# Kernel tuning notes

Hardware: AMD Instinct MI355X
Metric: run time of the kernel (lower is better)

Reference implementation:

```python
import jax, jax.numpy as jnp
import numpy as np

B, N, D, H = 32, 2048, 65, 64  # batch, seq_len, in_dim+out_dim, hid
GAMMA = 0.0001


def setup_inputs() -> dict:
    key = jax.random.key(0)
    kx, kq, kk, kv = jax.random.split(key, 4)
    x = jax.random.normal(kx, (B, N, D), dtype=jnp.float32)
    std_qk = (GAMMA / D) ** 0.5
    Wq = jax.random.normal(kq, (H, D), dtype=jnp.float32) * std_qk
    Wk = jax.random.normal(kk, (H, D), dtype=jnp.float32) * std_qk
    Wv = jax.random.normal(kv, (D, D), dtype=jnp.float32) * GAMMA
    return {"x": x, "Wq": Wq, "Wk": Wk, "Wv": Wv}


def reference(x, Wq, Wk, Wv):
    # Linear projections (torch nn.Linear: x @ W^T)
    Q = jnp.einsum('bnd,hd->bnh', x, Wq)  # [B, N, H]
    K = jnp.einsum('bnd,hd->bnh', x, Wk)  # [B, N, H]
    V = jnp.einsum('bnd,ed->bne', x, Wv)  # [B, N, D]
    # Non-softmax linear attention: (Q K^T) V, as written in the module
    scores = jnp.einsum('bnh,bmh->bnm', Q, K)  # [B, N, N]
    out = jnp.einsum('bnm,bmd->bnd', scores, V)  # [B, N, D]
    return out
```

## Files before the change

kernel.cpp:

```cpp
#include <hip/hip_runtime.h>

#define BB 32
#define NN 2048
#define DD 65
#define HH 64
#define ST 68
#define TILE (DD * ST)
#define CC 32

__device__ __forceinline__ float4 f4add(float4 a, float4 b) {
  return make_float4(a.x + b.x, a.y + b.y, a.z + b.z, a.w + b.w);
}

#define GL2LDS(g, l)                                             \
  __builtin_amdgcn_global_load_lds(                              \
      (const __attribute__((address_space(1))) void*)(g),        \
      (__attribute__((address_space(3))) void*)(l), 16, 0, 0)

__global__ __launch_bounds__(128, 2) void k1_gram(const float* __restrict__ x,
                                                  float* __restrict__ P) {
  __shared__ __align__(16) float Xl[2][64 * ST];
  const int t = (int)threadIdx.x;
  const int w = t >> 6, lane = t & 63;
  const int tx8 = lane & 7, ty8 = lane >> 3;
  const int chunk = (int)blockIdx.x * 2 + w;
  const int b = chunk >> 5, c = chunk & 31;
  const float4* src4 =
      (const float4*)(x + ((size_t)b * NN + (size_t)c * 64) * DD);
  float* Xw = Xl[w];

#pragma unroll
  for (int p = 0; p < 2; p++) {
    float4 tmp[9];
    const int cnt = p ? 8 : 9;
#pragma unroll
    for (int q = 0; q < 9; q++) {
      const int i4 = lane + 64 * (9 * p + q);
      if (q < cnt && i4 < 1040) tmp[q] = src4[i4];
    }
#pragma unroll
    for (int q = 0; q < 9; q++) {
      const int i4 = lane + 64 * (9 * p + q);
      if (q < cnt && i4 < 1040) {
        const int f = 4 * i4;
        const float vv[4] = {tmp[q].x, tmp[q].y, tmp[q].z, tmp[q].w};
#pragma unroll
        for (int j = 0; j < 4; j++) {
          const int r = (f + j) / DD, cc = (f + j) - r * DD;
          Xw[r * ST + cc] = vv[j];
        }
      }
    }
  }

  float g[8][8] = {};
  float f64[8] = {};
  float gcc = 0.f;
  for (int n = 0; n < 64; n++) {
    float rowf[8], colf[8];
    *(float4*)&rowf[0] = *(const float4*)&Xw[n * ST + 8 * ty8];
    *(float4*)&rowf[4] = *(const float4*)&Xw[n * ST + 8 * ty8 + 4];
    *(float4*)&colf[0] = *(const float4*)&Xw[n * ST + 8 * tx8];
    *(float4*)&colf[4] = *(const float4*)&Xw[n * ST + 8 * tx8 + 4];
    const float x64 = Xw[n * ST + 64];
#pragma unroll
    for (int r = 0; r < 8; r++)
#pragma unroll
      for (int cc = 0; cc < 8; cc++)
        g[r][cc] = fmaf(rowf[r], colf[cc], g[r][cc]);
#pragma unroll
    for (int cc = 0; cc < 8; cc++) f64[cc] = fmaf(x64, colf[cc], f64[cc]);
    gcc = fmaf(x64, x64, gcc);
  }

  float* Pp = P + (size_t)chunk * TILE;
#pragma unroll
  for (int r = 0; r < 8; r++) {
    *(float4*)&Pp[(8 * ty8 + r) * ST + 8 * tx8] = *(float4*)&g[r][0];
    *(float4*)&Pp[(8 * ty8 + r) * ST + 8 * tx8 + 4] = *(float4*)&g[r][4];
  }
  if (ty8 == 0) {
#pragma unroll
    for (int cc = 0; cc < 8; cc++) {
      Pp[64 * ST + 8 * tx8 + cc] = f64[cc];
      Pp[(8 * tx8 + cc) * ST + 64] = f64[cc];
    }
    if (tx8 == 0) Pp[64 * ST + 64] = gcc;
  }
}

__global__ __launch_bounds__(256) void kred(const float* __restrict__ P,
                                            float* __restrict__ G) {
  const int t = (int)threadIdx.x;
  const int blk = (int)blockIdx.x;
  const int b = blk / 5, s = blk - b * 5;
  const int Q = TILE / 4;
  const int i4 = s * 256 + t;
  if (i4 < Q) {
    const float4* Pb = (const float4*)(P + (size_t)b * CC * TILE);
    float4 acc = make_float4(0.f, 0.f, 0.f, 0.f);
#pragma unroll
    for (int grp = 0; grp < 4; grp++) {
      float4 v[8];
#pragma unroll
      for (int cc = 0; cc < 8; cc++)
        v[cc] = Pb[(size_t)(8 * grp + cc) * Q + i4];
#pragma unroll
      for (int stp = 4; stp >= 1; stp >>= 1)
#pragma unroll
        for (int cc = 0; cc < stp; cc++) v[cc] = f4add(v[cc], v[cc + stp]);
      acc = f4add(acc, v[0]);
    }
    ((float4*)(G + (size_t)b * TILE))[i4] = acc;
  }
}

__global__ __launch_bounds__(256) void k2_chain(
    const float* __restrict__ Wq, const float* __restrict__ Wk,
    const float* __restrict__ Wv, const float* __restrict__ G,
    float* __restrict__ Tm) {
  __shared__ __align__(16) float WqL[HH * ST];
  __shared__ __align__(16) float WkL[HH * ST];
  __shared__ __align__(16) float GL[TILE];
  __shared__ __align__(16) float WvT[TILE];
  __shared__ __align__(16) float Mr[8 * ST];
  __shared__ __align__(16) float Rr[8 * ST];

  const int t = (int)threadIdx.x;
  const int tx = t & 31, ty = t >> 5;
  const int blk = (int)blockIdx.x;
  const int b = blk / 9, rg = blk - b * 9;
  const int i = 8 * rg + ty;
  const bool alive = (i < DD);
  const int ic = alive ? i : 0;

  {
    float tq[17], tk[17];
#pragma unroll
    for (int q = 0; q < 17; q++) {
      const int idx = t + 256 * q;
      if (idx < HH * DD) { tq[q] = Wq[idx]; tk[q] = Wk[idx]; }
    }
#pragma unroll
    for (int q = 0; q < 17; q++) {
      const int idx = t + 256 * q;
      if (idx < HH * DD) {
        const int r = idx / DD, cc = idx - r * DD;
        WqL[r * ST + cc] = tq[q];
        WkL[r * ST + cc] = tk[q];
      }
    }
  }
  {
    const float4* Gb4 = (const float4*)(G + (size_t)b * TILE);
    float4 tG[5];
#pragma unroll
    for (int q = 0; q < 5; q++) {
      const int i4 = t + 256 * q;
      if (i4 < TILE / 4) tG[q] = Gb4[i4];
    }
#pragma unroll
    for (int q = 0; q < 5; q++) {
      const int i4 = t + 256 * q;
      if (i4 < TILE / 4) *((float4*)GL + i4) = tG[q];
    }
  }
  {
    float tv[17];
#pragma unroll
    for (int q = 0; q < 17; q++) {
      const int idx = t + 256 * q;
      if (idx < DD * DD) tv[q] = Wv[idx];
    }
#pragma unroll
    for (int q = 0; q < 17; q++) {
      const int idx = t + 256 * q;
      if (idx < DD * DD) {
        const int j = idx / DD, k = idx - j * DD;
        WvT[k * ST + j] = tv[q];
      }
    }
  }
  __syncthreads();

  {
    float m0 = 0.f, m1 = 0.f, m2 = 0.f;
    for (int h = 0; h < HH; h++) {
      const float wq = WqL[h * ST + ic];
      m0 = fmaf(wq, WkL[h * ST + tx], m0);
      m1 = fmaf(wq, WkL[h * ST + tx + 32], m1);
      m2 = fmaf(wq, WkL[h * ST + 64], m2);
    }
    if (alive) {
      Mr[ty * ST + tx] = m0;
      Mr[ty * ST + tx + 32] = m1;
      if (tx == 0) Mr[ty * ST + 64] = m2;
    }
  }
  __syncthreads();

  {
    float r0 = 0.f, r1 = 0.f, r2 = 0.f;
    for (int k = 0; k < DD; k++) {
      const float mm = Mr[ty * ST + k];
      r0 = fmaf(mm, GL[k * ST + tx], r0);
      r1 = fmaf(mm, GL[k * ST + tx + 32], r1);
      r2 = fmaf(mm, GL[k * ST + 64], r2);
    }
    if (alive) {
      Rr[ty * ST + tx] = r0;
      Rr[ty * ST + tx + 32] = r1;
      if (tx == 0) Rr[ty * ST + 64] = r2;
    }
  }
  __syncthreads();

  {
    float t0 = 0.f, t1 = 0.f, t2 = 0.f;
    for (int k = 0; k < DD; k++) {
      const float rv = Rr[ty * ST + k];
      t0 = fmaf(rv, WvT[k * ST + tx], t0);
      t1 = fmaf(rv, WvT[k * ST + tx + 32], t1);
      t2 = fmaf(rv, WvT[k * ST + 64], t2);
    }
    if (alive) {
      float* Tb = Tm + (size_t)b * TILE + (size_t)i * ST;
      Tb[tx] = t0;
      Tb[tx + 32] = t1;
      if (tx == 0) Tb[64] = t2;
    }
  }
}

__global__ __launch_bounds__(128, 2) void k3_out(const float* __restrict__ x,
                                                 const float* __restrict__ Tt,
                                                 float* __restrict__ out) {
  __shared__ __align__(16) float Tl[TILE];
  __shared__ __align__(16) float Xl[2][64 * ST];
  const int t = (int)threadIdx.x;
  const int w = t >> 6, lane = t & 63;
  const int tx8 = lane & 7, ty8 = lane >> 3;
  const int blk = (int)blockIdx.x;
  const int b = blk >> 4;
  const int chunk = (blk & 15) * 2 + w;
  const float4* Tg4 = (const float4*)(Tt + (size_t)b * TILE);
  const float4* src4 =
      (const float4*)(x + ((size_t)b * NN + (size_t)chunk * 64) * DD);
  float* Xw = Xl[w];

#pragma unroll
  for (int q = 0; q < 8; q++)
    GL2LDS(Tg4 + q * 128 + w * 64 + lane,
           Tl + (size_t)(q * 128 + w * 64) * 4);
  {
    const int s = 1024 + w * 64 + lane;
    if (s < TILE / 4) GL2LDS(Tg4 + s, Tl + (size_t)(1024 + w * 64) * 4);
  }

#pragma unroll
  for (int p = 0; p < 2; p++) {
    float4 tmp[9];
    const int cnt = p ? 8 : 9;
#pragma unroll
    for (int q = 0; q < 9; q++) {
      const int i4 = lane + 64 * (9 * p + q);
      if (q < cnt && i4 < 1040) tmp[q] = src4[i4];
    }
#pragma unroll
    for (int q = 0; q < 9; q++) {
      const int i4 = lane + 64 * (9 * p + q);
      if (q < cnt && i4 < 1040) {
        const int f = 4 * i4;
        const float vv[4] = {tmp[q].x, tmp[q].y, tmp[q].z, tmp[q].w};
#pragma unroll
        for (int j = 0; j < 4; j++) {
          const int r = (f + j) / DD, cc = (f + j) - r * DD;
          Xw[r * ST + cc] = vv[j];
        }
      }
    }
  }
  __syncthreads();

  float o[8][8] = {}, o64[8] = {};
  for (int kk = 0; kk < 64; kk += 4) {
    float xa[8][4];
#pragma unroll
    for (int r = 0; r < 8; r++)
      *(float4*)xa[r] = *(const float4*)&Xw[(8 * ty8 + r) * ST + kk];
#pragma unroll
    for (int e = 0; e < 4; e++) {
      float tb[8];
      *(float4*)&tb[0] = *(const float4*)&Tl[(kk + e) * ST + 8 * tx8];
      *(float4*)&tb[4] = *(const float4*)&Tl[(kk + e) * ST + 8 * tx8 + 4];
      const float t64 = Tl[(kk + e) * ST + 64];
#pragma unroll
      for (int r = 0; r < 8; r++) {
#pragma unroll
        for (int cc = 0; cc < 8; cc++)
          o[r][cc] = fmaf(xa[r][e], tb[cc], o[r][cc]);
        o64[r] = fmaf(xa[r][e], t64, o64[r]);
      }
    }
  }
  {
    float tb[8];
    *(float4*)&tb[0] = *(const float4*)&Tl[64 * ST + 8 * tx8];
    *(float4*)&tb[4] = *(const float4*)&Tl[64 * ST + 8 * tx8 + 4];
    const float t64 = Tl[64 * ST + 64];
#pragma unroll
    for (int r = 0; r < 8; r++) {
      const float xs = Xw[(8 * ty8 + r) * ST + 64];
#pragma unroll
      for (int cc = 0; cc < 8; cc++)
        o[r][cc] = fmaf(xs, tb[cc], o[r][cc]);
      o64[r] = fmaf(xs, t64, o64[r]);
    }
  }

  float* Ow = Xw;
#pragma unroll
  for (int r = 0; r < 8; r++) {
#pragma unroll
    for (int cc = 0; cc < 8; cc++)
      Ow[(8 * ty8 + r) * DD + 8 * tx8 + cc] = o[r][cc];
    if (tx8 == 0) Ow[(8 * ty8 + r) * DD + 64] = o64[r];
  }
  float4* ob4 = (float4*)(out + ((size_t)b * NN + (size_t)chunk * 64) * DD);
#pragma unroll
  for (int q = 0; q < 17; q++) {
    const int i4 = lane + 64 * q;
    if (i4 < 1040) ob4[i4] = ((const float4*)Ow)[i4];
  }
}

extern "C" void kernel_launch(void* const* d_in, const int* in_sizes, int n_in,
                              void* d_out, int out_size, void* d_ws,
                              size_t ws_size, hipStream_t stream) {
  const float* x = (const float*)d_in[0];
  const float* Wq = (const float*)d_in[1];
  const float* Wk = (const float*)d_in[2];
  const float* Wv = (const float*)d_in[3];
  float* out = (float*)d_out;

  float* P = (float*)d_ws;
  float* G = P + (size_t)BB * CC * TILE;
  float* Tm = G + (size_t)BB * TILE;

  k1_gram<<<BB * CC / 2, 128, 0, stream>>>(x, P);
  kred<<<BB * 5, 256, 0, stream>>>(P, G);
  k2_chain<<<BB * 9, 256, 0, stream>>>(Wq, Wk, Wv, G, Tm);
  k3_out<<<BB * CC / 2, 128, 0, stream>>>(x, Tm, out);
  (void)in_sizes; (void)n_in; (void)out_size; (void)ws_size;
}
```

Measured before the change: 127.8 us.

## Halve row chunks to 32, use 4-wave blocks, read x directly in output kernel

The Gram partial kernel now processes 32-row chunks with four waves per block, doubling the number of partial tiles and the reduction depth in kred. The output kernel drops the LDS staging of x and the LDS-based output transpose. Each lane reads its four x rows straight from global memory and writes results directly with unaligned scalar stores. The aim is more waves in flight and less LDS use per block, at the cost of a heavier partial-sum write and reduce and uncoalesced scalar global loads and stores in k3.

```diff
diff --git a/kernel.cpp b/kernel.cpp
--- a/kernel.cpp
+++ b/kernel.cpp
@@ -6,7 +6,8 @@
 #define HH 64
 #define ST 68
 #define TILE (DD * ST)
-#define CC 32
+#define CH 64
+#define CROWS 32
 
 __device__ __forceinline__ float4 f4add(float4 a, float4 b) {
   return make_float4(a.x + b.x, a.y + b.y, a.z + b.z, a.w + b.w);
@@ -17,31 +18,29 @@
       (const __attribute__((address_space(1))) void*)(g),        \
       (__attribute__((address_space(3))) void*)(l), 16, 0, 0)
 
-__global__ __launch_bounds__(128, 2) void k1_gram(const float* __restrict__ x,
+__global__ __launch_bounds__(256, 4) void k1_gram(const float* __restrict__ x,
                                                   float* __restrict__ P) {
-  __shared__ __align__(16) float Xl[2][64 * ST];
+  __shared__ __align__(16) float Xl[4][CROWS * ST];
   const int t = (int)threadIdx.x;
   const int w = t >> 6, lane = t & 63;
   const int tx8 = lane & 7, ty8 = lane >> 3;
-  const int chunk = (int)blockIdx.x * 2 + w;
-  const int b = chunk >> 5, c = chunk & 31;
+  const int ch = (int)blockIdx.x * 4 + w;
+  const int b = ch >> 6, c = ch & 63;
   const float4* src4 =
-      (const float4*)(x + ((size_t)b * NN + (size_t)c * 64) * DD);
+      (const float4*)(x + ((size_t)b * NN + (size_t)c * CROWS) * DD);
   float* Xw = Xl[w];
 
-#pragma unroll
-  for (int p = 0; p < 2; p++) {
+  {
     float4 tmp[9];
-    const int cnt = p ? 8 : 9;
 #pragma unroll
     for (int q = 0; q < 9; q++) {
-      const int i4 = lane + 64 * (9 * p + q);
-      if (q < cnt && i4 < 1040) tmp[q] = src4[i4];
+      const int i4 = lane + 64 * q;
+      if (i4 < 520) tmp[q] = src4[i4];
     }
 #pragma unroll
     for (int q = 0; q < 9; q++) {
-      const int i4 = lane + 64 * (9 * p + q);
-      if (q < cnt && i4 < 1040) {
+      const int i4 = lane + 64 * q;
+      if (i4 < 520) {
         const int f = 4 * i4;
         const float vv[4] = {tmp[q].x, tmp[q].y, tmp[q].z, tmp[q].w};
 #pragma unroll
@@ -56,7 +55,7 @@
   float g[8][8] = {};
   float f64[8] = {};
   float gcc = 0.f;
-  for (int n = 0; n < 64; n++) {
+  for (int n = 0; n < CROWS; n++) {
     float rowf[8], colf[8];
     *(float4*)&rowf[0] = *(const float4*)&Xw[n * ST + 8 * ty8];
     *(float4*)&rowf[4] = *(const float4*)&Xw[n * ST + 8 * ty8 + 4];
@@ -73,7 +72,7 @@
     gcc = fmaf(x64, x64, gcc);
   }
 
-  float* Pp = P + (size_t)chunk * TILE;
+  float* Pp = P + (size_t)ch * TILE;
 #pragma unroll
   for (int r = 0; r < 8; r++) {
     *(float4*)&Pp[(8 * ty8 + r) * ST + 8 * tx8] = *(float4*)&g[r][0];
@@ -97,10 +96,10 @@
   const int Q = TILE / 4;
   const int i4 = s * 256 + t;
   if (i4 < Q) {
-    const float4* Pb = (const float4*)(P + (size_t)b * CC * TILE);
+    const float4* Pb = (const float4*)(P + (size_t)b * CH * TILE);
     float4 acc = make_float4(0.f, 0.f, 0.f, 0.f);
 #pragma unroll
-    for (int grp = 0; grp < 4; grp++) {
+    for (int grp = 0; grp < 8; grp++) {
       float4 v[8];
 #pragma unroll
       for (int cc = 0; cc < 8; cc++)
@@ -232,70 +231,53 @@
   }
 }
 
-__global__ __launch_bounds__(128, 2) void k3_out(const float* __restrict__ x,
+__global__ __launch_bounds__(256, 4) void k3_out(const float* __restrict__ x,
                                                  const float* __restrict__ Tt,
                                                  float* __restrict__ out) {
   __shared__ __align__(16) float Tl[TILE];
-  __shared__ __align__(16) float Xl[2][64 * ST];
   const int t = (int)threadIdx.x;
   const int w = t >> 6, lane = t & 63;
-  const int tx8 = lane & 7, ty8 = lane >> 3;
+  const int tx8 = lane & 7, ry4 = lane >> 3;
   const int blk = (int)blockIdx.x;
   const int b = blk >> 4;
-  const int chunk = (blk & 15) * 2 + w;
+  const int c = (blk & 15) * 4 + w;
   const float4* Tg4 = (const float4*)(Tt + (size_t)b * TILE);
-  const float4* src4 =
-      (const float4*)(x + ((size_t)b * NN + (size_t)chunk * 64) * DD);
-  float* Xw = Xl[w];
-
-#pragma unroll
-  for (int q = 0; q < 8; q++)
-    GL2LDS(Tg4 + q * 128 + w * 64 + lane,
-           Tl + (size_t)(q * 128 + w * 64) * 4);
+  const float* xs = x + ((size_t)b * NN + (size_t)c * CROWS) * DD;
+
+#pragma unroll
+  for (int q = 0; q < 4; q++)
+    GL2LDS(Tg4 + q * 256 + w * 64 + lane,
+           Tl + (size_t)(q * 256 + w * 64) * 4);
   {
     const int s = 1024 + w * 64 + lane;
     if (s < TILE / 4) GL2LDS(Tg4 + s, Tl + (size_t)(1024 + w * 64) * 4);
   }
-
-#pragma unroll
-  for (int p = 0; p < 2; p++) {
-    float4 tmp[9];
-    const int cnt = p ? 8 : 9;
-#pragma unroll
-    for (int q = 0; q < 9; q++) {
-      const int i4 = lane + 64 * (9 * p + q);
-      if (q < cnt && i4 < 1040) tmp[q] = src4[i4];
-    }
-#pragma unroll
-    for (int q = 0; q < 9; q++) {
-      const int i4 = lane + 64 * (9 * p + q);
-      if (q < cnt && i4 < 1040) {
-        const int f = 4 * i4;
-        const float vv[4] = {tmp[q].x, tmp[q].y, tmp[q].z, tmp[q].w};
-#pragma unroll
-        for (int j = 0; j < 4; j++) {
-          const int r = (f + j) / DD, cc = (f + j) - r * DD;
-          Xw[r * ST + cc] = vv[j];
-        }
-      }
-    }
-  }
   __syncthreads();
 
-  float o[8][8] = {}, o64[8] = {};
+  const float* xr0 = xs + (size_t)(4 * ry4 + 0) * DD;
+  const float* xr1 = xs + (size_t)(4 * ry4 + 1) * DD;
+  const float* xr2 = xs + (size_t)(4 * ry4 + 2) * DD;
+  const float* xr3 = xs + (size_t)(4 * ry4 + 3) * DD;
+
+  float o[4][8] = {}, o64[4] = {};
   for (int kk = 0; kk < 64; kk += 4) {
-    float xa[8][4];
-#pragma unroll
-    for (int r = 0; r < 8; r++)
-      *(float4*)xa[r] = *(const float4*)&Xw[(8 * ty8 + r) * ST + kk];
+    float xa[4][4];
 #pragma unroll
     for (int e = 0; e < 4; e++) {
+      xa[0][e] = xr0[kk + e];
+      xa[1][e] = xr1[kk + e];
+      xa[2][e] = xr2[kk + e];
+      xa[3][e] = xr3[kk + e];
+    }
+#pragma unroll
+    for (int e = 0; e < 4; e++) {
+      const int k = kk + e;
       float tb[8];
-      *(float4*)&tb[0] = *(const float4*)&Tl[(kk + e) * ST + 8 * tx8];
-      *(float4*)&tb[4] = *(const float4*)&Tl[(kk + e) * ST + 8 * tx8 + 4];
-      const float t64 = Tl[(kk + e) * ST + 64];
-#pragma unroll
-      for (int r = 0; r < 8; r++) {
+      *(float4*)&tb[0] = *(const float4*)&Tl[k * ST + 8 * tx8];
+      *(float4*)&tb[4] = *(const float4*)&Tl[k * ST + 8 * tx8 + 4];
+      const float t64 = Tl[k * ST + 64];
+#pragma unroll
+      for (int r = 0; r < 4; r++) {
 #pragma unroll
         for (int cc = 0; cc < 8; cc++)
           o[r][cc] = fmaf(xa[r][e], tb[cc], o[r][cc]);
@@ -304,33 +286,33 @@
     }
   }
   {
+    float xk[4];
+    xk[0] = xr0[64]; xk[1] = xr1[64]; xk[2] = xr2[64]; xk[3] = xr3[64];
     float tb[8];
     *(float4*)&tb[0] = *(const float4*)&Tl[64 * ST + 8 * tx8];
     *(float4*)&tb[4] = *(const float4*)&Tl[64 * ST + 8 * tx8 + 4];
     const float t64 = Tl[64 * ST + 64];
 #pragma unroll
-    for (int r = 0; r < 8; r++) {
-      const float xs = Xw[(8 * ty8 + r) * ST + 64];
+    for (int r = 0; r < 4; r++) {
 #pragma unroll
       for (int cc = 0; cc < 8; cc++)
-        o[r][cc] = fmaf(xs, tb[cc], o[r][cc]);
-      o64[r] = fmaf(xs, t64, o64[r]);
-    }
-  }
-
-  float* Ow = Xw;
-#pragma unroll
-  for (int r = 0; r < 8; r++) {
+        o[r][cc] = fmaf(xk[r], tb[cc], o[r][cc]);
+      o64[r] = fmaf(xk[r], t64, o64[r]);
+    }
+  }
+
+  float* ob = out + ((size_t)b * NN + (size_t)c * CROWS) * DD;
+#pragma unroll
+  for (int r = 0; r < 4; r++) {
+    const int row = 4 * ry4 + r;
 #pragma unroll
     for (int cc = 0; cc < 8; cc++)
-      Ow[(8 * ty8 + r) * DD + 8 * tx8 + cc] = o[r][cc];
-    if (tx8 == 0) Ow[(8 * ty8 + r) * DD + 64] = o64[r];
-  }
-  float4* ob4 = (float4*)(out + ((size_t)b * NN + (size_t)chunk * 64) * DD);
-#pragma unroll
-  for (int q = 0; q < 17; q++) {
-    const int i4 = lane + 64 * q;
-    if (i4 < 1040) ob4[i4] = ((const float4*)Ow)[i4];
+      ob[row * DD + 8 * tx8 + cc] = o[r][cc];
+  }
+  if (tx8 == 0) {
+#pragma unroll
+    for (int r = 0; r < 4; r++)
+      ob[(4 * ry4 + r) * DD + 64] = o64[r];
   }
 }
 
@@ -344,12 +326,12 @@
   float* out = (float*)d_out;
 
   float* P = (float*)d_ws;
-  float* G = P + (size_t)BB * CC * TILE;
+  float* G = P + (size_t)BB * CH * TILE;
   float* Tm = G + (size_t)BB * TILE;
 
-  k1_gram<<<BB * CC / 2, 128, 0, stream>>>(x, P);
+  k1_gram<<<BB * CH / 4, 256, 0, stream>>>(x, P);
   kred<<<BB * 5, 256, 0, stream>>>(P, G);
   k2_chain<<<BB * 9, 256, 0, stream>>>(Wq, Wk, Wv, G, Tm);
-  k3_out<<<BB * CC / 2, 128, 0, stream>>>(x, Tm, out);
+  k3_out<<<BB * CH / 4, 256, 0, stream>>>(x, Tm, out);
   (void)in_sizes; (void)n_in; (void)out_size; (void)ws_size;
 }
```

Result: faster. 121.4 us (-5.0%).
